# Kernel optimization log

Hardware: AMD Instinct MI355X
Metric: run time of the kernel (lower is better)

## Reference

```python
import jax, jax.numpy as jnp
import numpy as np

V, T, E, HID = 32000, 48, 128, 256
B, L = 256, 512
H = HID // 2  # per-direction LSTM hidden


def setup_inputs() -> dict:
    key = jax.random.key(0)
    ks = jax.random.split(key, 16)
    lengths = jax.random.randint(ks[0], (B,), L // 2, L + 1)
    mask = (jnp.arange(L)[None, :] < lengths[:, None])  # (B, L) bool, step 0 always on
    words = jax.random.randint(ks[1], (B, L), 1, V).astype(jnp.int32)
    words = jnp.where(mask, words, 0)  # padding_idx = 0
    tags = jax.random.randint(ks[2], (B, L), 0, T).astype(jnp.int32)
    s = 0.1
    emb = jax.random.normal(ks[3], (V, E), jnp.float32) * s
    emb = emb.at[0].set(0.0)  # padding_idx row zeroed
    Wih_f = jax.random.normal(ks[4], (4 * H, E), jnp.float32) * s
    Whh_f = jax.random.normal(ks[5], (4 * H, H), jnp.float32) * s
    bih_f = jax.random.normal(ks[6], (4 * H,), jnp.float32) * s
    bhh_f = jax.random.normal(ks[7], (4 * H,), jnp.float32) * s
    Wih_b = jax.random.normal(ks[8], (4 * H, E), jnp.float32) * s
    Whh_b = jax.random.normal(ks[9], (4 * H, H), jnp.float32) * s
    bih_b = jax.random.normal(ks[10], (4 * H,), jnp.float32) * s
    bhh_b = jax.random.normal(ks[11], (4 * H,), jnp.float32) * s
    Wout = jax.random.normal(ks[12], (T, HID), jnp.float32) * s
    bout = jax.random.normal(ks[13], (T,), jnp.float32) * s
    trans = jax.random.normal(ks[14], (T, T), jnp.float32) * s
    se = jax.random.normal(ks[15], (2, T), jnp.float32) * s
    return dict(words=words, tags=tags, mask=mask, emb=emb,
                Wih_f=Wih_f, Whh_f=Whh_f, bih_f=bih_f, bhh_f=bhh_f,
                Wih_b=Wih_b, Whh_b=Whh_b, bih_b=bih_b, bhh_b=bhh_b,
                Wout=Wout, bout=bout, trans=trans,
                start_trans=se[0], end_trans=se[1])


def _lstm_dir(x, Wih, Whh, bih, bhh, reverse):
    # x: (L, B, E) -> hs: (L, B, H); PyTorch gate order i, f, g, o
    Lx, Bx, _ = x.shape
    Hx = Whh.shape[1]
    def step(carry, xt):
        h, c = carry
        g = xt @ Wih.T + h @ Whh.T + (bih + bhh)
        i, f, gg, o = jnp.split(g, 4, axis=-1)
        c = jax.nn.sigmoid(f) * c + jax.nn.sigmoid(i) * jnp.tanh(gg)
        h = jax.nn.sigmoid(o) * jnp.tanh(c)
        return (h, c), h
    init = (jnp.zeros((Bx, Hx), x.dtype), jnp.zeros((Bx, Hx), x.dtype))
    _, hs = jax.lax.scan(step, init, x, reverse=reverse)
    return hs


def reference(words, tags, mask, emb, Wih_f, Whh_f, bih_f, bhh_f,
              Wih_b, Whh_b, bih_b, bhh_b, Wout, bout, trans,
              start_trans, end_trans):
    Bn = words.shape[0]
    # --- features: embedding -> BiLSTM -> linear ---
    x = emb[words].transpose(1, 0, 2)          # (L, B, E)
    h_f = _lstm_dir(x, Wih_f, Whh_f, bih_f, bhh_f, reverse=False)
    h_b = _lstm_dir(x, Wih_b, Whh_b, bih_b, bhh_b, reverse=True)
    h = jnp.concatenate([h_f, h_b], axis=-1)   # (L, B, 2H)
    emis = h @ Wout.T + bout                   # (L, B, T)
    mT = mask.T                                # (L, B) bool
    mF = mT.astype(emis.dtype)
    tT = tags.T.astype(jnp.int32)              # (L, B)

    # --- CRF numerator: score of gold path ---
    barange = jnp.arange(Bn)
    num0 = start_trans[tT[0]] + emis[0, barange, tT[0]]
    def num_step(score, inp):
        em_t, tag_prev, tag_t, m_t = inp
        step_score = trans[tag_prev, tag_t] + em_t[barange, tag_t]
        return score + step_score * m_t, None
    num, _ = jax.lax.scan(num_step, num0, (emis[1:], tT[:-1], tT[1:], mF[1:]))
    seq_ends = mF.sum(0).astype(jnp.int32) - 1
    last_tags = tT[seq_ends, barange]
    num = num + end_trans[last_tags]

    # --- CRF denominator: forward algorithm (logsumexp recurrence) ---
    den0 = start_trans[None, :] + emis[0]      # (B, T)
    def den_step(score, inp):
        em_t, m_t = inp
        nxt = jax.nn.logsumexp(score[:, :, None] + trans[None] + em_t[:, None, :], axis=1)
        return jnp.where(m_t[:, None], nxt, score), None
    den, _ = jax.lax.scan(den_step, den0, (emis[1:], mT[1:]))
    denom = jax.nn.logsumexp(den + end_trans[None, :], axis=1)

    llh = num - denom
    return -llh.mean()  # reduction='mean', negated
```

## Files before the change

kernel.cpp:

```cpp
#include <hip/hip_runtime.h>
#include <hip/hip_bf16.h>

typedef unsigned short ushort_t;
typedef unsigned int uint_t;
typedef __bf16 bf16x8 __attribute__((ext_vector_type(8)));
typedef float f32x4 __attribute__((ext_vector_type(4)));
typedef float f32x16 __attribute__((ext_vector_type(16)));

#define L2E 1.44269504088896340736f
#define LN2 0.69314718055994530942f

#define WGBAR() __asm__ volatile("s_waitcnt lgkmcnt(0)\n\ts_barrier" ::: "memory")

static __device__ __forceinline__ float fexp2(float x) { return __builtin_amdgcn_exp2f(x); }
static __device__ __forceinline__ float flog2(float x) { return __builtin_amdgcn_logf(x); }
static __device__ __forceinline__ float frcp (float x) { return __builtin_amdgcn_rcpf(x); }

static __device__ __forceinline__ float sigm(float x) {
  return frcp(1.0f + fexp2(-L2E * x));
}
static __device__ __forceinline__ float tanha(float x) {
  return 1.0f - 2.0f * frcp(1.0f + fexp2(2.0f * L2E * x));
}

static __device__ __forceinline__ uint_t cvtpk(float lo, float hi) {
  uint_t r;
  asm("v_cvt_pk_bf16_f32 %0, %1, %2" : "=v"(r) : "v"(lo), "v"(hi));
  return r;
}
static __device__ __forceinline__ bf16x8 pack8(float4 a, float4 b) {
  uint4 u = make_uint4(cvtpk(a.x, a.y), cvtpk(a.z, a.w),
                       cvtpk(b.x, b.y), cvtpk(b.z, b.w));
  return __builtin_bit_cast(bf16x8, u);
}
static __device__ __forceinline__ bf16x8 zero8() {
  uint4 z = make_uint4(0u, 0u, 0u, 0u);
  return __builtin_bit_cast(bf16x8, z);
}
static __device__ __forceinline__ uint2 pack4(float4 a) {
  return make_uint2(cvtpk(a.x, a.y), cvtpk(a.z, a.w));
}

template <int K>
static __device__ __forceinline__ float rotk(float x) {
  if constexpr (K == 0) {
    return x;
  } else {
    return __builtin_bit_cast(float, __builtin_amdgcn_update_dpp(
        0, __builtin_bit_cast(int, x), 0x120 + K, 0xf, 0xf, true));
  }
}

__global__ __launch_bounds__(512, 2) void k2_lstm(
    const int* __restrict__ words, const float* __restrict__ emb,
    const float* __restrict__ Wih_f, const float* __restrict__ Whh_f,
    const float* __restrict__ bih_f, const float* __restrict__ bhh_f,
    const float* __restrict__ Wih_b, const float* __restrict__ Whh_b,
    const float* __restrict__ bih_b, const float* __restrict__ bhh_b,
    ushort_t* __restrict__ h_f, ushort_t* __restrict__ h_b) {
  const int wg = blockIdx.x;
  const int dir = wg >> 7;
  const int r0 = (wg & 127) << 1;
  const float* Whh = dir ? Whh_b : Whh_f;
  const float* Wih = dir ? Wih_b : Wih_f;
  const float* bih = dir ? bih_b : bih_f;
  const float* bhh = dir ? bhh_b : bhh_f;
  ushort_t* hout = dir ? h_b : h_f;

  const int tid = threadIdx.x;
  const int w = tid >> 6;
  const int lane = tid & 63;
  const int l15 = lane & 15;
  const int kq = lane >> 4;

  __shared__ __align__(16) ushort_t hx[2][2][136];
  __shared__ __align__(16) ushort_t xp[2][16][128][4];
  __shared__ __align__(16) ushort_t xs[2][16][136];

  bf16x8 wfh[4][4], wfx[4][4];
  float biasP[4];
#pragma unroll
  for (int Q = 0; Q < 4; ++Q) {
    const int n = Q * 128 + w * 16 + l15;
    biasP[Q] = bih[n] + bhh[n];
#pragma unroll
    for (int c = 0; c < 4; ++c) {
      const int k0 = c * 32 + kq * 8;
      const float* sh = Whh + n * 128 + k0;
      const float* sx = Wih + n * 128 + k0;
      wfh[Q][c] = pack8(*(const float4*)sh, *(const float4*)(sh + 4));
      wfx[Q][c] = pack8(*(const float4*)sx, *(const float4*)(sx + 4));
    }
  }

  const int ur = (lane >> 4) & 1;
  const int uj = w * 16 + l15;
  float cst = 0.f;
  const f32x4 fz = {0.f, 0.f, 0.f, 0.f};

  const int sm = tid >> 5;
  const int sc = (tid & 31) * 4;
  const int str = r0 + (sm & 1);
  const int stl = sm >> 1;

  uint_t pd0[4], pd1[4];
  f32x4 pc = {0.f, 0.f, 0.f, 0.f};
  f32x4 pcsv = {0.f, 0.f, 0.f, 0.f};

  if (tid < 256) hx[0][tid >> 7][tid & 127] = 0;
  {
    const int tg = stl;
    const int tf = dir ? (511 - tg) : tg;
    const int word = words[str * 512 + tf];
    float4 av = *(const float4*)(emb + (size_t)word * 128 + sc);
    *(uint2*)&xs[1][sm][sc] = pack4(av);
  }
  WGBAR();
  {
    f32x4 qv[4];
#pragma unroll
    for (int Q = 0; Q < 4; ++Q) {
      f32x4 pc0 = {biasP[Q], biasP[Q], biasP[Q], biasP[Q]};
#pragma unroll
      for (int c = 0; c < 4; ++c) {
        bf16x8 af = __builtin_bit_cast(bf16x8, *(const uint4*)&xs[1][l15][kq * 8 + c * 32]);
        pc0 = __builtin_amdgcn_mfma_f32_16x16x32_bf16(af, wfx[Q][c], pc0, 0, 0, 0);
      }
      qv[Q] = pc0;
    }
#pragma unroll
    for (int rr = 0; rr < 4; ++rr) {
      pd0[rr] = cvtpk(qv[0][rr], qv[1][rr]);
      pd1[rr] = cvtpk(qv[2][rr], qv[3][rr]);
      *(uint2*)&xp[0][kq * 4 + rr][uj][0] = make_uint2(pd0[rr], pd1[rr]);
    }
  }
  {
    const int tg = 8 + stl;
    const int tf = dir ? (511 - tg) : tg;
    const int word = words[str * 512 + tf];
    float4 av = *(const float4*)(emb + (size_t)word * 128 + sc);
    *(uint2*)&xs[0][sm][sc] = pack4(av);
  }
  WGBAR();

  int sword = 0;
  float4 se0 = make_float4(0.f, 0.f, 0.f, 0.f);

#pragma unroll 1
  for (int i = 0; i < 64; ++i) {
    const int pcon = i & 1;
    const int ppro = pcon ^ 1;
    bf16x8 afp[4];
    if (i < 63) {
#pragma unroll
      for (int c = 0; c < 4; ++c)
        afp[c] = __builtin_bit_cast(bf16x8, *(const uint4*)&xs[pcon][l15][kq * 8 + c * 32]);
    }
#pragma unroll
    for (int s = 0; s < 8; ++s) {
      const int t = i * 8 + s;
      const int p = t & 1;
      const uint2 xq = *(const uint2*)&xp[pcon][2 * s + ur][uj][0];
      if (i < 62) {
        if (s == 0) {
          const int tg = (i + 2) * 8 + stl;
          const int tf = dir ? (511 - tg) : tg;
          sword = words[str * 512 + tf];
        }
        if (s == 2) se0 = *(const float4*)(emb + (size_t)sword * 128 + sc);
        if (s == 6) *(uint2*)&xs[ppro][sm][sc] = pack4(se0);
      }
      f32x4 a0, a1, a2, a3;
      const ushort_t* abase = &hx[p][l15 & 1][kq * 8];
      {
        bf16x8 af = __builtin_bit_cast(bf16x8, *(const uint4*)(abase));
        a0 = __builtin_amdgcn_mfma_f32_16x16x32_bf16(af, wfh[0][0], fz, 0, 0, 0);
        a1 = __builtin_amdgcn_mfma_f32_16x16x32_bf16(af, wfh[1][0], fz, 0, 0, 0);
        a2 = __builtin_amdgcn_mfma_f32_16x16x32_bf16(af, wfh[2][0], fz, 0, 0, 0);
        a3 = __builtin_amdgcn_mfma_f32_16x16x32_bf16(af, wfh[3][0], fz, 0, 0, 0);
      }
#pragma unroll
      for (int c = 1; c < 4; ++c) {
        bf16x8 af = __builtin_bit_cast(bf16x8, *(const uint4*)(abase + c * 32));
        a0 = __builtin_amdgcn_mfma_f32_16x16x32_bf16(af, wfh[0][c], a0, 0, 0, 0);
        a1 = __builtin_amdgcn_mfma_f32_16x16x32_bf16(af, wfh[1][c], a1, 0, 0, 0);
        a2 = __builtin_amdgcn_mfma_f32_16x16x32_bf16(af, wfh[2][c], a2, 0, 0, 0);
        a3 = __builtin_amdgcn_mfma_f32_16x16x32_bf16(af, wfh[3][c], a3, 0, 0, 0);
      }
      if (i < 63) {
        const int Q = s >> 1;
        if ((s & 1) == 0) {
          pc = f32x4{biasP[Q], biasP[Q], biasP[Q], biasP[Q]};
          pc = __builtin_amdgcn_mfma_f32_16x16x32_bf16(afp[0], wfx[Q][0], pc, 0, 0, 0);
          pc = __builtin_amdgcn_mfma_f32_16x16x32_bf16(afp[1], wfx[Q][1], pc, 0, 0, 0);
        } else {
          pc = __builtin_amdgcn_mfma_f32_16x16x32_bf16(afp[2], wfx[Q][2], pc, 0, 0, 0);
          pc = __builtin_amdgcn_mfma_f32_16x16x32_bf16(afp[3], wfx[Q][3], pc, 0, 0, 0);
          if ((s & 2) == 0) {
            pcsv = pc;
          } else if (s == 3) {
#pragma unroll
            for (int rr = 0; rr < 4; ++rr) pd0[rr] = cvtpk(pcsv[rr], pc[rr]);
          } else {
#pragma unroll
            for (int rr = 0; rr < 4; ++rr) {
              pd1[rr] = cvtpk(pcsv[rr], pc[rr]);
              *(uint2*)&xp[ppro][kq * 4 + rr][uj][0] = make_uint2(pd0[rr], pd1[rr]);
            }
          }
        }
      }
      const float g0 = (ur ? a0[1] : a0[0]) + __builtin_bit_cast(float, xq.x << 16);
      const float g1 = (ur ? a1[1] : a1[0]) + __builtin_bit_cast(float, xq.x & 0xffff0000u);
      const float g2 = (ur ? a2[1] : a2[0]) + __builtin_bit_cast(float, xq.y << 16);
      const float g3 = (ur ? a3[1] : a3[0]) + __builtin_bit_cast(float, xq.y & 0xffff0000u);
      const float si = sigm(g0), sf = sigm(g1), so = sigm(g3);
      const float tg = tanha(g2);
      cst = sf * cst + si * tg;
      const float h = so * tanha(cst);
      const ushort_t hb = (ushort_t)cvtpk(h, h);
      if (lane < 32) {
        hx[p ^ 1][ur][uj] = hb;
        const int tf = dir ? (511 - t) : t;
        hout[(tf * 256 + r0 + ur) * 128 + uj] = hb;
      }
      WGBAR();
    }
  }
}

__global__ __launch_bounds__(256, 2) void k3_emis(
    const ushort_t* __restrict__ h_f, const ushort_t* __restrict__ h_b,
    const float* __restrict__ Wout, const float* __restrict__ bout,
    float* __restrict__ emis, float* __restrict__ loss_out) {
  if (blockIdx.x == 0 && threadIdx.x == 0) loss_out[0] = 0.f;
  const int w = threadIdx.x >> 6;
  const int lane = threadIdx.x & 63;
  const int m31 = lane & 31;
  const int q = lane >> 5;
  const int Mbase = blockIdx.x * 128 + w * 32;

  bf16x8 bfr[2][16];
  float bo[2];
#pragma unroll
  for (int T = 0; T < 2; ++T) {
    const int n = T * 32 + m31;
    if (n < 48) {
      bo[T] = bout[n];
#pragma unroll
      for (int c = 0; c < 16; ++c) {
        const float* src = Wout + n * 256 + c * 16 + q * 8;
        bfr[T][c] = pack8(*(const float4*)src, *(const float4*)(src + 4));
      }
    } else {
      bo[T] = 0.f;
#pragma unroll
      for (int c = 0; c < 16; ++c) bfr[T][c] = zero8();
    }
  }
  f32x16 acc0{}, acc1{};
  const ushort_t* hrf = h_f + (long)(Mbase + m31) * 128;
  const ushort_t* hrb = h_b + (long)(Mbase + m31) * 128;
#pragma unroll
  for (int c = 0; c < 16; ++c) {
    const ushort_t* src = (c < 8) ? (hrf + c * 16 + q * 8) : (hrb + (c - 8) * 16 + q * 8);
    bf16x8 af = __builtin_bit_cast(bf16x8, *(const uint4*)src);
    acc0 = __builtin_amdgcn_mfma_f32_32x32x16_bf16(af, bfr[0][c], acc0, 0, 0, 0);
    acc1 = __builtin_amdgcn_mfma_f32_32x32x16_bf16(af, bfr[1][c], acc1, 0, 0, 0);
  }
#pragma unroll
  for (int T = 0; T < 2; ++T) {
    const int n = T * 32 + m31;
    if (n >= 48) continue;
    f32x16 A = T ? acc1 : acc0;
#pragma unroll
    for (int r = 0; r < 16; ++r) {
      const int row = (r & 3) + ((r >> 2) << 3) + (q << 2);
      emis[(long)(Mbase + row) * 48 + n] = A[r] + bo[T];
    }
  }
}

#define K4_ROW(OP, m) \
  OP(m, 0) OP(m, 1) OP(m, 2) OP(m, 3) OP(m, 4) OP(m, 5) OP(m, 6) OP(m, 7) \
  OP(m, 8) OP(m, 9) OP(m, 10) OP(m, 11) OP(m, 12) OP(m, 13) OP(m, 14) OP(m, 15)
#define K4_ALL(OP) K4_ROW(OP, 0) K4_ROW(OP, 1) K4_ROW(OP, 2) K4_ROW(OP, 3)

#define ROTMOD_0  ""
#define ROTMOD_1  "row_ror:1 row_mask:0xf bank_mask:0xf"
#define ROTMOD_2  "row_ror:2 row_mask:0xf bank_mask:0xf"
#define ROTMOD_3  "row_ror:3 row_mask:0xf bank_mask:0xf"
#define ROTMOD_4  "row_ror:4 row_mask:0xf bank_mask:0xf"
#define ROTMOD_5  "row_ror:5 row_mask:0xf bank_mask:0xf"
#define ROTMOD_6  "row_ror:6 row_mask:0xf bank_mask:0xf"
#define ROTMOD_7  "row_ror:7 row_mask:0xf bank_mask:0xf"
#define ROTMOD_8  "row_ror:8 row_mask:0xf bank_mask:0xf"
#define ROTMOD_9  "row_ror:9 row_mask:0xf bank_mask:0xf"
#define ROTMOD_10 "row_ror:10 row_mask:0xf bank_mask:0xf"
#define ROTMOD_11 "row_ror:11 row_mask:0xf bank_mask:0xf"
#define ROTMOD_12 "row_ror:12 row_mask:0xf bank_mask:0xf"
#define ROTMOD_13 "row_ror:13 row_mask:0xf bank_mask:0xf"
#define ROTMOD_14 "row_ror:14 row_mask:0xf bank_mask:0xf"
#define ROTMOD_15 "row_ror:15 row_mask:0xf bank_mask:0xf"

#define K4_FMA(m_, k_) asm( \
    "v_fmac_f32 %0, %1, %2 " ROTMOD_##k_ \
    : "+v"(acc[((m_) * 16 + (k_)) & 7]) \
    : "v"(dm[m_]), "v"(pcr[(m_) * 16 + (k_)]));

#define K4_BODY(FOLD, LOADSTMT, ENSRC, MBIT, MEAS)                            \
  {                                                                           \
    float E = Ecur;                                                           \
    int eApp = 0;                                                             \
    if (FOLD) {                                                               \
      const float sc_ =                                                       \
          __builtin_bit_cast(float, (uint_t)(127 - e_pend) << 23);            \
      E *= sc_;                                                               \
      eApp = e_pend;                                                          \
    }                                                                         \
    LOADSTMT;                                                                 \
    const float En = fexp2((ENSRC) * L2E);                                    \
    float dm[4];                                                              \
    dm[0] = d;                                                                \
    dm[1] = __shfl_xor(d, 16, 64);                                            \
    dm[2] = __shfl_xor(d, 32, 64);                                            \
    dm[3] = __shfl_xor(d, 48, 64);                                            \
    float acc[8] = {0.f, 0.f, 0.f, 0.f, 0.f, 0.f, 0.f, 0.f};                  \
    K4_ALL(K4_FMA)                                                            \
    const float nxt = (((acc[0] + acc[1]) + (acc[2] + acc[3])) +              \
                       ((acc[4] + acc[5]) + (acc[6] + acc[7]))) * E;          \
    if (MBIT) {                                                               \
      d = v ? nxt : 0.f;                                                      \
      S += eApp;                                                              \
    }                                                                         \
    if (MEAS) {                                                               \
      const int db_ =                                                         \
          __builtin_amdgcn_readfirstlane(__builtin_bit_cast(int, d));         \
      e_pend = ((db_ >> 23) & 0xff) - 127;                                    \
    }                                                                         \
    Ecur = En;                                                                \
  }

__global__ __launch_bounds__(128, 1) void k4_crf(
    const int* __restrict__ words, const int* __restrict__ tags,
    const float* __restrict__ emis, const float* __restrict__ trans,
    const float* __restrict__ st, const float* __restrict__ et,
    float* __restrict__ out) {
  const int b = blockIdx.x;
  const int tid = threadIdx.x;
  const int j = tid & 63;
  __shared__ float res[2];

  if (tid >= 64) {
    float s = 0.f;
    int cnt = 0;
#pragma unroll 1
    for (int s8 = 0; s8 < 8; ++s8) {
      const int t = j + (s8 << 6);
      const int wv = words[b * 512 + t];
      const int tg = tags[b * 512 + t];
      const bool mt = (wv != 0);
      cnt += mt ? 1 : 0;
      if (t == 0) {
        s += st[tg] + emis[b * 48 + tg];
      } else if (mt) {
        const int tp = tags[b * 512 + t - 1];
        s += trans[tp * 48 + tg] + emis[(t * 256 + b) * 48 + tg];
      }
    }
#pragma unroll
    for (int d = 32; d; d >>= 1) {
      s += __shfl_xor(s, d, 64);
      cnt += __shfl_xor(cnt, d, 64);
    }
    if (j == 0) {
      const int lt = tags[b * 512 + cnt - 1];
      res[1] = s + et[lt];
    }
  } else {
    const bool v = j < 48;
    const int jj = v ? j : 47;

    float pcr[64];
    {
      float pm[4];
      const float pj = (float)j;
      pm[0] = pj;
      pm[1] = __shfl_xor(pj, 16, 64);
      pm[2] = __shfl_xor(pj, 32, 64);
      pm[3] = __shfl_xor(pj, 48, 64);
#define K4_CAL(m, k) { const int idx_ = (int)rotk<k>(pm[m]); \
      pcr[(m) * 16 + (k)] = (v && idx_ < 48) ? fexp2(trans[idx_ * 48 + j] * L2E) : 0.f; }
      K4_ALL(K4_CAL)
#undef K4_CAL
    }

    unsigned long long mb[8];
#pragma unroll
    for (int q = 0; q < 8; ++q)
      mb[q] = __ballot(words[b * 512 + q * 64 + j] != 0);

    float d = v ? fexp2((st[j] + emis[b * 48 + j]) * L2E) : 0.f;
    int S = 0, e_pend = 0;

    const float* __restrict__ eb = emis + jj;
#define EMLD(tt) eb[(size_t)((tt) * 256 + b) * 48]

    float pm_0 = EMLD(1), pm_1 = EMLD(2), pm_2 = EMLD(3), pm_3 = EMLD(4);
    float pm_4 = EMLD(5), pm_5 = EMLD(6), pm_6 = EMLD(7);
    float em_0 = EMLD(8),  em_1 = EMLD(9),  em_2 = EMLD(10), em_3 = EMLD(11);
    float em_4 = EMLD(12), em_5 = EMLD(13), em_6 = EMLD(14), em_7 = EMLD(15);
    float Ecur = fexp2(pm_0 * L2E);

    {
      const uint_t mm = (uint_t)mb[0];
      K4_BODY(false, (void)0, pm_1, (mm >> 1) & 1u, false)
      K4_BODY(true,  (void)0, pm_2, (mm >> 2) & 1u, false)
      K4_BODY(false, (void)0, pm_3, (mm >> 3) & 1u, false)
      K4_BODY(false, (void)0, pm_4, (mm >> 4) & 1u, false)
      K4_BODY(false, (void)0, pm_5, (mm >> 5) & 1u, false)
      K4_BODY(false, (void)0, pm_6, (mm >> 6) & 1u, false)
      K4_BODY(false, (void)0, em_0, (mm >> 7) & 1u, false)
    }

#pragma unroll 1
    for (int q = 0; q < 8; ++q) {
      const unsigned long long mq =
          q == 0 ? mb[0] : q == 1 ? mb[1] : q == 2 ? mb[2] : q == 3 ? mb[3] :
          q == 4 ? mb[4] : q == 5 ? mb[5] : q == 6 ? mb[6] : mb[7];
#pragma unroll 1
      for (int gi = (q == 0 ? 1 : 0); gi < 8; ++gi) {
        const int G = q * 64 + gi * 8;
        const uint_t mm = (uint_t)(mq >> (gi * 8));
        const int Lb = G + 8;
        K4_BODY(false, em_0 = EMLD(min(511, Lb + 0)), em_1, (mm >> 0) & 1u, true)
        K4_BODY(false, em_1 = EMLD(min(511, Lb + 1)), em_2, (mm >> 1) & 1u, false)
        K4_BODY(true,  em_2 = EMLD(min(511, Lb + 2)), em_3, (mm >> 2) & 1u, false)
        K4_BODY(false, em_3 = EMLD(min(511, Lb + 3)), em_4, (mm >> 3) & 1u, false)
        K4_BODY(false, em_4 = EMLD(min(511, Lb + 4)), em_5, (mm >> 4) & 1u, false)
        K4_BODY(false, em_5 = EMLD(min(511, Lb + 5)), em_6, (mm >> 5) & 1u, false)
        K4_BODY(false, em_6 = EMLD(min(511, Lb + 6)), em_7, (mm >> 6) & 1u, false)
        K4_BODY(false, em_7 = EMLD(min(511, Lb + 7)), em_0, (mm >> 7) & 1u, false)
      }
    }
#undef EMLD

    float uf = v ? d * fexp2(et[j] * L2E) : 0.f;
#pragma unroll
    for (int dd = 32; dd; dd >>= 1) uf += __shfl_xor(uf, dd, 64);
    if (j == 0) res[0] = ((float)S + flog2(uf)) * LN2;
  }
  __syncthreads();
  if (tid == 0) atomicAdd(out, (res[0] - res[1]) * (1.0f / 256.0f));
}

extern "C" void kernel_launch(void* const* d_in, const int* in_sizes, int n_in,
                              void* d_out, int out_size, void* d_ws, size_t ws_size,
                              hipStream_t stream) {
  (void)in_sizes; (void)n_in; (void)out_size; (void)ws_size;
  const int*   words = (const int*)d_in[0];
  const int*   tags  = (const int*)d_in[1];
  const float* emb   = (const float*)d_in[3];
  const float* Wih_f = (const float*)d_in[4];
  const float* Whh_f = (const float*)d_in[5];
  const float* bih_f = (const float*)d_in[6];
  const float* bhh_f = (const float*)d_in[7];
  const float* Wih_b = (const float*)d_in[8];
  const float* Whh_b = (const float*)d_in[9];
  const float* bih_b = (const float*)d_in[10];
  const float* bhh_b = (const float*)d_in[11];
  const float* Wout  = (const float*)d_in[12];
  const float* bout  = (const float*)d_in[13];
  const float* trans = (const float*)d_in[14];
  const float* st    = (const float*)d_in[15];
  const float* et    = (const float*)d_in[16];

  char* ws = (char*)d_ws;
  ushort_t* h_f   = (ushort_t*)(ws);
  ushort_t* h_b   = (ushort_t*)(ws + 33554432);
  float*    emis  = (float*)   (ws + 67108864);

  k2_lstm <<<256, 512, 0, stream>>>(words, emb,
                                    Wih_f, Whh_f, bih_f, bhh_f,
                                    Wih_b, Whh_b, bih_b, bhh_b,
                                    h_f, h_b);
  k3_emis <<<1024, 256, 0, stream>>>(h_f, h_b, Wout, bout, emis, (float*)d_out);
  k4_crf  <<<256, 128, 0, stream>>>(words, tags, emis, trans, st, et, (float*)d_out);
}
```

Before: 550.2 us.

## Fuse emission projection into CRF kernel with batch-major hidden layout

Removes the separate emission GEMM kernel. The LSTM now writes hidden states in a batch-major interleaved layout (batch, time, 256), and the CRF kernel computes each 64-step emission tile with MFMA into double-buffered shared memory while wave 0 runs the forward recurrence. This drops one launch and the emis round-trip through global memory, and lets emission loads come from LDS instead of strided global reads. In exchange the CRF kernel now does the projection work, adds per-tile block barriers, and the LSTM's scattered stores change pattern.

```diff
diff --git a/kernel.cpp b/kernel.cpp
--- a/kernel.cpp
+++ b/kernel.cpp
@@ -5,7 +5,6 @@
 typedef unsigned int uint_t;
 typedef __bf16 bf16x8 __attribute__((ext_vector_type(8)));
 typedef float f32x4 __attribute__((ext_vector_type(4)));
-typedef float f32x16 __attribute__((ext_vector_type(16)));
 
 #define L2E 1.44269504088896340736f
 #define LN2 0.69314718055994530942f
@@ -32,10 +31,6 @@
   uint4 u = make_uint4(cvtpk(a.x, a.y), cvtpk(a.z, a.w),
                        cvtpk(b.x, b.y), cvtpk(b.z, b.w));
   return __builtin_bit_cast(bf16x8, u);
-}
-static __device__ __forceinline__ bf16x8 zero8() {
-  uint4 z = make_uint4(0u, 0u, 0u, 0u);
-  return __builtin_bit_cast(bf16x8, z);
 }
 static __device__ __forceinline__ uint2 pack4(float4 a) {
   return make_uint2(cvtpk(a.x, a.y), cvtpk(a.z, a.w));
@@ -57,15 +52,15 @@
     const float* __restrict__ bih_f, const float* __restrict__ bhh_f,
     const float* __restrict__ Wih_b, const float* __restrict__ Whh_b,
     const float* __restrict__ bih_b, const float* __restrict__ bhh_b,
-    ushort_t* __restrict__ h_f, ushort_t* __restrict__ h_b) {
+    ushort_t* __restrict__ hT, float* __restrict__ loss_out) {
   const int wg = blockIdx.x;
   const int dir = wg >> 7;
   const int r0 = (wg & 127) << 1;
+  if (wg == 0 && threadIdx.x == 0) loss_out[0] = 0.f;
   const float* Whh = dir ? Whh_b : Whh_f;
   const float* Wih = dir ? Wih_b : Wih_f;
   const float* bih = dir ? bih_b : bih_f;
   const float* bhh = dir ? bhh_b : bhh_f;
-  ushort_t* hout = dir ? h_b : h_f;
 
   const int tid = threadIdx.x;
   const int w = tid >> 6;
@@ -223,61 +218,9 @@
       if (lane < 32) {
         hx[p ^ 1][ur][uj] = hb;
         const int tf = dir ? (511 - t) : t;
-        hout[(tf * 256 + r0 + ur) * 128 + uj] = hb;
+        hT[((size_t)(r0 + ur) * 512 + tf) * 256 + (dir << 7) + uj] = hb;
       }
       WGBAR();
-    }
-  }
-}
-
-__global__ __launch_bounds__(256, 2) void k3_emis(
-    const ushort_t* __restrict__ h_f, const ushort_t* __restrict__ h_b,
-    const float* __restrict__ Wout, const float* __restrict__ bout,
-    float* __restrict__ emis, float* __restrict__ loss_out) {
-  if (blockIdx.x == 0 && threadIdx.x == 0) loss_out[0] = 0.f;
-  const int w = threadIdx.x >> 6;
-  const int lane = threadIdx.x & 63;
-  const int m31 = lane & 31;
-  const int q = lane >> 5;
-  const int Mbase = blockIdx.x * 128 + w * 32;
-
-  bf16x8 bfr[2][16];
-  float bo[2];
-#pragma unroll
-  for (int T = 0; T < 2; ++T) {
-    const int n = T * 32 + m31;
-    if (n < 48) {
-      bo[T] = bout[n];
-#pragma unroll
-      for (int c = 0; c < 16; ++c) {
-        const float* src = Wout + n * 256 + c * 16 + q * 8;
-        bfr[T][c] = pack8(*(const float4*)src, *(const float4*)(src + 4));
-      }
-    } else {
-      bo[T] = 0.f;
-#pragma unroll
-      for (int c = 0; c < 16; ++c) bfr[T][c] = zero8();
-    }
-  }
-  f32x16 acc0{}, acc1{};
-  const ushort_t* hrf = h_f + (long)(Mbase + m31) * 128;
-  const ushort_t* hrb = h_b + (long)(Mbase + m31) * 128;
-#pragma unroll
-  for (int c = 0; c < 16; ++c) {
-    const ushort_t* src = (c < 8) ? (hrf + c * 16 + q * 8) : (hrb + (c - 8) * 16 + q * 8);
-    bf16x8 af = __builtin_bit_cast(bf16x8, *(const uint4*)src);
-    acc0 = __builtin_amdgcn_mfma_f32_32x32x16_bf16(af, bfr[0][c], acc0, 0, 0, 0);
-    acc1 = __builtin_amdgcn_mfma_f32_32x32x16_bf16(af, bfr[1][c], acc1, 0, 0, 0);
-  }
-#pragma unroll
-  for (int T = 0; T < 2; ++T) {
-    const int n = T * 32 + m31;
-    if (n >= 48) continue;
-    f32x16 A = T ? acc1 : acc0;
-#pragma unroll
-    for (int r = 0; r < 16; ++r) {
-      const int row = (r & 3) + ((r >> 2) << 3) + (q << 2);
-      emis[(long)(Mbase + row) * 48 + n] = A[r] + bo[T];
     }
   }
 }
@@ -342,114 +285,171 @@
     Ecur = En;                                                                \
   }
 
-__global__ __launch_bounds__(128, 1) void k4_crf(
+#define EMLDS(tt) emis_t[((tt) >> 6) & 1][(tt) & 63][jj]
+
+__global__ __launch_bounds__(128, 1) void k4_fused(
     const int* __restrict__ words, const int* __restrict__ tags,
-    const float* __restrict__ emis, const float* __restrict__ trans,
+    const ushort_t* __restrict__ hT, const float* __restrict__ Wout,
+    const float* __restrict__ bout, const float* __restrict__ trans,
     const float* __restrict__ st, const float* __restrict__ et,
     float* __restrict__ out) {
   const int b = blockIdx.x;
   const int tid = threadIdx.x;
-  const int j = tid & 63;
+  const int wv = tid >> 6;
+  const int lane = tid & 63;
+  const int l15 = lane & 15;
+  const int kq = lane >> 4;
+
+  __shared__ __align__(16) ushort_t wfrag[3][8][64][8];
+  __shared__ float emis_t[2][64][50];
   __shared__ float res[2];
 
-  if (tid >= 64) {
-    float s = 0.f;
-    int cnt = 0;
+  const ushort_t* hb_base = hT + (size_t)b * 512 * 256;
+
+  float bo3[3];
+#pragma unroll
+  for (int jt = 0; jt < 3; ++jt) bo3[jt] = bout[jt * 16 + l15];
 #pragma unroll 1
-    for (int s8 = 0; s8 < 8; ++s8) {
-      const int t = j + (s8 << 6);
-      const int wv = words[b * 512 + t];
+  for (int f = wv; f < 24; f += 2) {
+    const int jt = f >> 3, c = f & 7;
+    const float* src = Wout + (jt * 16 + l15) * 256 + c * 32 + kq * 8;
+    bf16x8 fr = pack8(*(const float4*)src, *(const float4*)(src + 4));
+    *(uint4*)&wfrag[jt][c][lane][0] = __builtin_bit_cast(uint4, fr);
+  }
+
+  const int j = lane;
+  const bool v = j < 48;
+  const int jj = v ? j : 47;
+  float pcr[64];
+  unsigned long long mb0, mb1, mb2, mb3, mb4, mb5, mb6, mb7;
+  float s_num = 0.f;
+  int cnt = 0;
+  if (wv == 0) {
+    float pm[4];
+    const float pj = (float)j;
+    pm[0] = pj;
+    pm[1] = __shfl_xor(pj, 16, 64);
+    pm[2] = __shfl_xor(pj, 32, 64);
+    pm[3] = __shfl_xor(pj, 48, 64);
+#define K4_CAL(m, k) { const int idx_ = (int)rotk<k>(pm[m]); \
+    pcr[(m) * 16 + (k)] = (v && idx_ < 48) ? fexp2(trans[idx_ * 48 + j] * L2E) : 0.f; }
+    K4_ALL(K4_CAL)
+#undef K4_CAL
+    mb0 = __ballot(words[b * 512 + 0 * 64 + j] != 0);
+    mb1 = __ballot(words[b * 512 + 1 * 64 + j] != 0);
+    mb2 = __ballot(words[b * 512 + 2 * 64 + j] != 0);
+    mb3 = __ballot(words[b * 512 + 3 * 64 + j] != 0);
+    mb4 = __ballot(words[b * 512 + 4 * 64 + j] != 0);
+    mb5 = __ballot(words[b * 512 + 5 * 64 + j] != 0);
+    mb6 = __ballot(words[b * 512 + 6 * 64 + j] != 0);
+    mb7 = __ballot(words[b * 512 + 7 * 64 + j] != 0);
+  }
+  __syncthreads();
+
+  auto produce = [&](int tile) {
+    const int t0 = tile * 64;
+    const int buf = tile & 1;
+#pragma unroll
+    for (int tsn = 0; tsn < 2; ++tsn) {
+      const int ts = wv * 2 + tsn;
+      const int tt0 = t0 + ts * 16;
+      bf16x8 afr[8];
+#pragma unroll
+      for (int c = 0; c < 8; ++c)
+        afr[c] = __builtin_bit_cast(bf16x8,
+            *(const uint4*)(hb_base + (size_t)(tt0 + l15) * 256 + c * 32 + kq * 8));
+#pragma unroll
+      for (int jt = 0; jt < 3; ++jt) {
+        f32x4 acc2 = {bo3[jt], bo3[jt], bo3[jt], bo3[jt]};
+#pragma unroll
+        for (int c = 0; c < 8; ++c) {
+          bf16x8 bfr = __builtin_bit_cast(bf16x8, *(const uint4*)&wfrag[jt][c][lane][0]);
+          acc2 = __builtin_amdgcn_mfma_f32_16x16x32_bf16(afr[c], bfr, acc2, 0, 0, 0);
+        }
+#pragma unroll
+        for (int r = 0; r < 4; ++r)
+          emis_t[buf][ts * 16 + kq * 4 + r][jt * 16 + l15] = acc2[r];
+      }
+    }
+  };
+
+  produce(0);
+  __syncthreads();
+
+  float d = 0.f, Ecur = 0.f;
+  int S = 0, e_pend = 0;
+  float pm_0, pm_1, pm_2, pm_3, pm_4, pm_5, pm_6;
+  float em_0, em_1, em_2, em_3, em_4, em_5, em_6, em_7;
+
+#pragma unroll 1
+  for (int p = 0; p < 8; ++p) {
+    if (p < 7) produce(p + 1);
+    __syncthreads();
+    if (wv == 0) {
+      const unsigned long long mq =
+          p == 0 ? mb0 : p == 1 ? mb1 : p == 2 ? mb2 : p == 3 ? mb3 :
+          p == 4 ? mb4 : p == 5 ? mb5 : p == 6 ? mb6 : mb7;
+      if (p == 0) {
+        d = v ? fexp2((st[j] + EMLDS(0)) * L2E) : 0.f;
+        pm_0 = EMLDS(1); pm_1 = EMLDS(2); pm_2 = EMLDS(3); pm_3 = EMLDS(4);
+        pm_4 = EMLDS(5); pm_5 = EMLDS(6); pm_6 = EMLDS(7);
+        em_0 = EMLDS(8);  em_1 = EMLDS(9);  em_2 = EMLDS(10); em_3 = EMLDS(11);
+        em_4 = EMLDS(12); em_5 = EMLDS(13); em_6 = EMLDS(14); em_7 = EMLDS(15);
+        Ecur = fexp2(pm_0 * L2E);
+        const uint_t mm = (uint_t)mq;
+        K4_BODY(false, (void)0, pm_1, (mm >> 1) & 1u, false)
+        K4_BODY(true,  (void)0, pm_2, (mm >> 2) & 1u, false)
+        K4_BODY(false, (void)0, pm_3, (mm >> 3) & 1u, false)
+        K4_BODY(false, (void)0, pm_4, (mm >> 4) & 1u, false)
+        K4_BODY(false, (void)0, pm_5, (mm >> 5) & 1u, false)
+        K4_BODY(false, (void)0, pm_6, (mm >> 6) & 1u, false)
+        K4_BODY(false, (void)0, em_0, (mm >> 7) & 1u, false)
+      }
+#pragma unroll 1
+      for (int gi = (p == 0 ? 1 : 0); gi < 8; ++gi) {
+        const int G = p * 64 + gi * 8;
+        const uint_t mm = (uint_t)(mq >> (gi * 8));
+        const int Lb = G + 8;
+        K4_BODY(false, em_0 = EMLDS(min(511, Lb + 0)), em_1, (mm >> 0) & 1u, true)
+        K4_BODY(false, em_1 = EMLDS(min(511, Lb + 1)), em_2, (mm >> 1) & 1u, false)
+        K4_BODY(true,  em_2 = EMLDS(min(511, Lb + 2)), em_3, (mm >> 2) & 1u, false)
+        K4_BODY(false, em_3 = EMLDS(min(511, Lb + 3)), em_4, (mm >> 3) & 1u, false)
+        K4_BODY(false, em_4 = EMLDS(min(511, Lb + 4)), em_5, (mm >> 4) & 1u, false)
+        K4_BODY(false, em_5 = EMLDS(min(511, Lb + 5)), em_6, (mm >> 5) & 1u, false)
+        K4_BODY(false, em_6 = EMLDS(min(511, Lb + 6)), em_7, (mm >> 6) & 1u, false)
+        K4_BODY(false, em_7 = EMLDS(min(511, Lb + 7)), em_0, (mm >> 7) & 1u, false)
+      }
+    } else {
+      const int t = p * 64 + lane;
+      const int wvd = words[b * 512 + t];
       const int tg = tags[b * 512 + t];
-      const bool mt = (wv != 0);
+      const bool mt = (wvd != 0);
       cnt += mt ? 1 : 0;
       if (t == 0) {
-        s += st[tg] + emis[b * 48 + tg];
+        s_num += st[tg] + emis_t[0][0][tg];
       } else if (mt) {
         const int tp = tags[b * 512 + t - 1];
-        s += trans[tp * 48 + tg] + emis[(t * 256 + b) * 48 + tg];
-      }
-    }
-#pragma unroll
-    for (int d = 32; d; d >>= 1) {
-      s += __shfl_xor(s, d, 64);
-      cnt += __shfl_xor(cnt, d, 64);
-    }
-    if (j == 0) {
-      const int lt = tags[b * 512 + cnt - 1];
-      res[1] = s + et[lt];
-    }
-  } else {
-    const bool v = j < 48;
-    const int jj = v ? j : 47;
-
-    float pcr[64];
-    {
-      float pm[4];
-      const float pj = (float)j;
-      pm[0] = pj;
-      pm[1] = __shfl_xor(pj, 16, 64);
-      pm[2] = __shfl_xor(pj, 32, 64);
-      pm[3] = __shfl_xor(pj, 48, 64);
-#define K4_CAL(m, k) { const int idx_ = (int)rotk<k>(pm[m]); \
-      pcr[(m) * 16 + (k)] = (v && idx_ < 48) ? fexp2(trans[idx_ * 48 + j] * L2E) : 0.f; }
-      K4_ALL(K4_CAL)
-#undef K4_CAL
-    }
-
-    unsigned long long mb[8];
-#pragma unroll
-    for (int q = 0; q < 8; ++q)
-      mb[q] = __ballot(words[b * 512 + q * 64 + j] != 0);
-
-    float d = v ? fexp2((st[j] + emis[b * 48 + j]) * L2E) : 0.f;
-    int S = 0, e_pend = 0;
-
-    const float* __restrict__ eb = emis + jj;
-#define EMLD(tt) eb[(size_t)((tt) * 256 + b) * 48]
-
-    float pm_0 = EMLD(1), pm_1 = EMLD(2), pm_2 = EMLD(3), pm_3 = EMLD(4);
-    float pm_4 = EMLD(5), pm_5 = EMLD(6), pm_6 = EMLD(7);
-    float em_0 = EMLD(8),  em_1 = EMLD(9),  em_2 = EMLD(10), em_3 = EMLD(11);
-    float em_4 = EMLD(12), em_5 = EMLD(13), em_6 = EMLD(14), em_7 = EMLD(15);
-    float Ecur = fexp2(pm_0 * L2E);
-
-    {
-      const uint_t mm = (uint_t)mb[0];
-      K4_BODY(false, (void)0, pm_1, (mm >> 1) & 1u, false)
-      K4_BODY(true,  (void)0, pm_2, (mm >> 2) & 1u, false)
-      K4_BODY(false, (void)0, pm_3, (mm >> 3) & 1u, false)
-      K4_BODY(false, (void)0, pm_4, (mm >> 4) & 1u, false)
-      K4_BODY(false, (void)0, pm_5, (mm >> 5) & 1u, false)
-      K4_BODY(false, (void)0, pm_6, (mm >> 6) & 1u, false)
-      K4_BODY(false, (void)0, em_0, (mm >> 7) & 1u, false)
-    }
-
-#pragma unroll 1
-    for (int q = 0; q < 8; ++q) {
-      const unsigned long long mq =
-          q == 0 ? mb[0] : q == 1 ? mb[1] : q == 2 ? mb[2] : q == 3 ? mb[3] :
-          q == 4 ? mb[4] : q == 5 ? mb[5] : q == 6 ? mb[6] : mb[7];
-#pragma unroll 1
-      for (int gi = (q == 0 ? 1 : 0); gi < 8; ++gi) {
-        const int G = q * 64 + gi * 8;
-        const uint_t mm = (uint_t)(mq >> (gi * 8));
-        const int Lb = G + 8;
-        K4_BODY(false, em_0 = EMLD(min(511, Lb + 0)), em_1, (mm >> 0) & 1u, true)
-        K4_BODY(false, em_1 = EMLD(min(511, Lb + 1)), em_2, (mm >> 1) & 1u, false)
-        K4_BODY(true,  em_2 = EMLD(min(511, Lb + 2)), em_3, (mm >> 2) & 1u, false)
-        K4_BODY(false, em_3 = EMLD(min(511, Lb + 3)), em_4, (mm >> 3) & 1u, false)
-        K4_BODY(false, em_4 = EMLD(min(511, Lb + 4)), em_5, (mm >> 4) & 1u, false)
-        K4_BODY(false, em_5 = EMLD(min(511, Lb + 5)), em_6, (mm >> 5) & 1u, false)
-        K4_BODY(false, em_6 = EMLD(min(511, Lb + 6)), em_7, (mm >> 6) & 1u, false)
-        K4_BODY(false, em_7 = EMLD(min(511, Lb + 7)), em_0, (mm >> 7) & 1u, false)
-      }
-    }
-#undef EMLD
-
+        s_num += trans[tp * 48 + tg] + emis_t[p & 1][t & 63][tg];
+      }
+    }
+    __syncthreads();
+  }
+
+  if (wv == 0) {
     float uf = v ? d * fexp2(et[j] * L2E) : 0.f;
 #pragma unroll
     for (int dd = 32; dd; dd >>= 1) uf += __shfl_xor(uf, dd, 64);
     if (j == 0) res[0] = ((float)S + flog2(uf)) * LN2;
+  } else {
+#pragma unroll
+    for (int dd = 32; dd; dd >>= 1) {
+      s_num += __shfl_xor(s_num, dd, 64);
+      cnt += __shfl_xor(cnt, dd, 64);
+    }
+    if (lane == 0) {
+      const int lt = tags[b * 512 + cnt - 1];
+      res[1] = s_num + et[lt];
+    }
   }
   __syncthreads();
   if (tid == 0) atomicAdd(out, (res[0] - res[1]) * (1.0f / 256.0f));
@@ -477,14 +477,12 @@
   const float* et    = (const float*)d_in[16];
 
   char* ws = (char*)d_ws;
-  ushort_t* h_f   = (ushort_t*)(ws);
-  ushort_t* h_b   = (ushort_t*)(ws + 33554432);
-  float*    emis  = (float*)   (ws + 67108864);
-
-  k2_lstm <<<256, 512, 0, stream>>>(words, emb,
-                                    Wih_f, Whh_f, bih_f, bhh_f,
-                                    Wih_b, Whh_b, bih_b, bhh_b,
-                                    h_f, h_b);
-  k3_emis <<<1024, 256, 0, stream>>>(h_f, h_b, Wout, bout, emis, (float*)d_out);
-  k4_crf  <<<256, 128, 0, stream>>>(words, tags, emis, trans, st, et, (float*)d_out);
-}
+  ushort_t* h_T = (ushort_t*)(ws);
+
+  k2_lstm  <<<256, 512, 0, stream>>>(words, emb,
+                                     Wih_f, Whh_f, bih_f, bhh_f,
+                                     Wih_b, Whh_b, bih_b, bhh_b,
+                                     h_T, (float*)d_out);
+  k4_fused <<<256, 128, 0, stream>>>(words, tags, h_T, Wout, bout,
+                                     trans, st, et, (float*)d_out);
+}
```

Measured after the change: 501.1 us. -8.9%, faster.
